# Kernel tuning notes

Measured on AMD Instinct MI355X. Metric: run time of the kernel, lower is better.

Reference implementation:

```python
import jax, jax.numpy as jnp
import numpy as np

BS, L, D, N = 4, 2048, 1024, 16

def setup_inputs() -> dict:
    key = jax.random.key(0)
    ks = jax.random.split(key, 8)
    s = 1.0 / np.sqrt(D)
    x  = jax.random.normal(ks[0], (BS, L, D), dtype=jnp.float32)
    # torch Linear params; stored transposed so y = x @ W + b
    W1 = jax.random.uniform(ks[1], (D, D), jnp.float32, -s, s)
    b1 = jax.random.uniform(ks[2], (D,),   jnp.float32, -s, s)
    W2 = jax.random.uniform(ks[3], (D, N), jnp.float32, -s, s)
    b2 = jax.random.uniform(ks[4], (N,),   jnp.float32, -s, s)
    W3 = jax.random.uniform(ks[5], (D, N), jnp.float32, -s, s)
    b3 = jax.random.uniform(ks[6], (N,),   jnp.float32, -s, s)
    A  = jax.random.normal(ks[7], (D, N),  jnp.float32) * np.sqrt(2.0 / (D + N))  # xavier
    return {"x": x, "W1": W1, "b1": b1, "W2": W2, "b2": b2, "W3": W3, "b3": b3, "A": A}

def reference(x, W1, b1, W2, b2, W3, b3, A):
    # S6 forward (non-recurrent branch).
    B = x @ W2 + b2                     # (b,l,n)
    C = x @ W3 + b3                     # (b,l,n)
    delta = jax.nn.softplus(x @ W1 + b1)  # (b,l,d)
    # dA = exp(einsum('bld,dn->bldn', delta, A)) is multiplied by an all-zero h
    # in the original forward, so it does not affect the output (dead code under DCE).
    dB = jnp.einsum('bld,bln->bldn', delta, B)   # (b,l,d,n) -- 512 MB intermediate
    h = x[..., None] * dB                         # (b,l,d,n)
    y = jnp.einsum('bln,bldn->bld', C, h)         # (b,l,d)
    return y
```

## Files before the change

### kernel.cpp

```cpp
#include <hip/hip_runtime.h>
#include <hip/hip_bf16.h>
#include <math.h>


namespace {

constexpr int Dd   = 1024;
constexpr int ROWS = 8192;

typedef __bf16 bf16x8 __attribute__((ext_vector_type(8)));
typedef float  floatx4 __attribute__((ext_vector_type(4)));

__device__ __forceinline__ float softplus_fast(float v) {
    float l = __logf(1.0f + __expf(v));
    return v > 15.0f ? v : l;
}
__device__ __forceinline__ float bf_lo(unsigned short u) {
    union { unsigned q; float f; } c; c.q = ((unsigned)u) << 16; return c.f;
}

__device__ __forceinline__ void gld_lds16(const __bf16* g, __bf16* l) {
    __builtin_amdgcn_global_load_lds(
        (const __attribute__((address_space(1))) void*)g,
        (__attribute__((address_space(3))) void*)l, 16, 0, 0);
}

#define BAR()    asm volatile("s_barrier" ::: "memory")
#define LGKM0()  asm volatile("s_waitcnt lgkmcnt(0)" ::: "memory")
#define VMCNT(n) asm volatile("s_waitcnt vmcnt(" #n ")" ::: "memory")

__global__ __launch_bounds__(256) void w23_kernel(
    const float* __restrict__ W2, const float* __restrict__ W3,
    __bf16* __restrict__ W2t, __bf16* __restrict__ W3t)
{
    const int t  = threadIdx.x;
    const int n  = t >> 4;
    const int k0 = blockIdx.x * 64 + (t & 15) * 4;
    ushort4 a, b;
    union { __bf16 h; unsigned short u; } c;
    c.h = (__bf16)W2[(size_t)(k0 + 0) * 16 + n]; a.x = c.u;
    c.h = (__bf16)W2[(size_t)(k0 + 1) * 16 + n]; a.y = c.u;
    c.h = (__bf16)W2[(size_t)(k0 + 2) * 16 + n]; a.z = c.u;
    c.h = (__bf16)W2[(size_t)(k0 + 3) * 16 + n]; a.w = c.u;
    c.h = (__bf16)W3[(size_t)(k0 + 0) * 16 + n]; b.x = c.u;
    c.h = (__bf16)W3[(size_t)(k0 + 1) * 16 + n]; b.y = c.u;
    c.h = (__bf16)W3[(size_t)(k0 + 2) * 16 + n]; b.z = c.u;
    c.h = (__bf16)W3[(size_t)(k0 + 3) * 16 + n]; b.w = c.u;
    *(ushort4*)&W2t[(size_t)n * Dd + k0] = a;
    *(ushort4*)&W3t[(size_t)n * Dd + k0] = b;
}

__global__ __launch_bounds__(256, 4) void prep_kernel(
    const float* __restrict__ X, const float* __restrict__ W1,
    const __bf16* __restrict__ W2t, const float* __restrict__ b2,
    const __bf16* __restrict__ W3t, const float* __restrict__ b3,
    __bf16* __restrict__ Xb, __bf16* __restrict__ W1t, float* __restrict__ Sv)
{
    const int t = threadIdx.x;

    if (blockIdx.x >= 512) {
        __shared__ __bf16 tile[64][66];
        const int bidx = blockIdx.x - 512;
        const int bi = bidx >> 4, bj = bidx & 15;
        const int c = t & 63, r4 = t >> 6;
        #pragma unroll
        for (int i = 0; i < 16; ++i) {
            const int r = i * 4 + r4;
            tile[r][c] = (__bf16)W1[(size_t)(bi * 64 + r) * Dd + bj * 64 + c];
        }
        __syncthreads();
        #pragma unroll
        for (int i = 0; i < 16; ++i) {
            const int r = i * 4 + r4;
            W1t[(size_t)(bj * 64 + r) * Dd + bi * 64 + c] = tile[c][r];
        }
        return;
    }

    __shared__ float red[4][2][16][16];
    const int w = t >> 6, lane = t & 63;
    const int l15 = lane & 15, quad = lane >> 4;
    const int row0 = blockIdx.x * 16;
    const int kw = w * 256;
    const size_t xoff = (size_t)(row0 + l15) * Dd;
    const size_t woff = (size_t)l15 * Dd;

    floatx4 acc0 = {0.f, 0.f, 0.f, 0.f}, acc1 = {0.f, 0.f, 0.f, 0.f};
    #pragma unroll
    for (int ks = 0; ks < 8; ++ks) {
        const int k0 = kw + ks * 32 + quad * 8;
        const float4 xa = *(const float4*)&X[xoff + k0];
        const float4 xb = *(const float4*)&X[xoff + k0 + 4];
        bf16x8 af;
        af[0] = (__bf16)xa.x; af[1] = (__bf16)xa.y;
        af[2] = (__bf16)xa.z; af[3] = (__bf16)xa.w;
        af[4] = (__bf16)xb.x; af[5] = (__bf16)xb.y;
        af[6] = (__bf16)xb.z; af[7] = (__bf16)xb.w;
        *(bf16x8*)&Xb[xoff + k0] = af;
        const bf16x8 w2f = *(const bf16x8*)&W2t[woff + k0];
        const bf16x8 w3f = *(const bf16x8*)&W3t[woff + k0];
        acc0 = __builtin_amdgcn_mfma_f32_16x16x32_bf16(af, w2f, acc0, 0, 0, 0);
        acc1 = __builtin_amdgcn_mfma_f32_16x16x32_bf16(af, w3f, acc1, 0, 0, 0);
    }
    #pragma unroll
    for (int r = 0; r < 4; ++r) {
        red[w][0][quad * 4 + r][l15] = acc0[r];
        red[w][1][quad * 4 + r][l15] = acc1[r];
    }
    __syncthreads();
    {
        const int r = t >> 4, n = t & 15;
        float B = b2[n], C = b3[n];
        #pragma unroll
        for (int ww = 0; ww < 4; ++ww) {
            B += red[ww][0][r][n];
            C += red[ww][1][r][n];
        }
        float p = B * C;
        p += __shfl_xor(p, 1); p += __shfl_xor(p, 2);
        p += __shfl_xor(p, 4); p += __shfl_xor(p, 8);
        if (n == 0) Sv[row0 + r] = p;
    }
}

#define MF(mt, nt, a_, b_) \
    acc[mt][nt] = __builtin_amdgcn_mfma_f32_16x16x32_bf16(a_, b_, acc[mt][nt], 0, 0, 0)
#define MFMA8(mb) do { \
    __builtin_amdgcn_s_setprio(1); \
    MF(mb + 0, 0, af0, bf0); MF(mb + 0, 1, af0, bf1); \
    MF(mb + 1, 0, af1, bf0); MF(mb + 1, 1, af1, bf1); \
    MF(mb + 2, 0, af2, bf0); MF(mb + 2, 1, af2, bf1); \
    MF(mb + 3, 0, af3, bf0); MF(mb + 3, 1, af3, bf1); \
    __builtin_amdgcn_s_setprio(0); } while (0)

#define TILE(B0_, B1_, NX1_, KA_, KB_, S1_, S2_, N1_, N2_) do { \
    bf16x8 af0, af1, af2, af3, bf0, bf1; \
     \
    af0 = rdA(B0_, 0); af1 = rdA(B0_, 1); af2 = rdA(B0_, 2); af3 = rdA(B0_, 3); \
    bf0 = rdB(B0_, 0); bf1 = rdB(B0_, 1); \
    if (S1_) { stageA(NX1_, KA_); stageB(NX1_, KA_); } \
    BAR(); LGKM0(); MFMA8(0); BAR(); \
     \
    af0 = rdA(B0_, 4); af1 = rdA(B0_, 5); af2 = rdA(B0_, 6); af3 = rdA(B0_, 7); \
    BAR(); LGKM0(); MFMA8(4); VMCNT(N1_); BAR(); \
     \
    af0 = rdA(B1_, 0); af1 = rdA(B1_, 1); af2 = rdA(B1_, 2); af3 = rdA(B1_, 3); \
    bf0 = rdB(B1_, 0); bf1 = rdB(B1_, 1); \
    if (S2_) { stageA(B0_, KB_); stageB(B0_, KB_); } \
    BAR(); LGKM0(); MFMA8(0); BAR(); \
     \
    af0 = rdA(B1_, 4); af1 = rdA(B1_, 5); af2 = rdA(B1_, 6); af3 = rdA(B1_, 7); \
    BAR(); LGKM0(); MFMA8(4); VMCNT(N2_); BAR(); \
} while (0)

__global__ __launch_bounds__(512, 2) void gemm_kernel(
    const __bf16* __restrict__ Xb, const __bf16* __restrict__ W1t,
    const float* __restrict__ Sv, const float* __restrict__ b1,
    float* __restrict__ Y)
{
    __shared__ __attribute__((aligned(16))) __bf16 lds[73728];
    const int t = threadIdx.x, lane = t & 63;
    const int w = t >> 6, wm = w & 1, wn = w >> 1;
    const int l15 = lane & 15, quad = lane >> 4;
    const int cb = blockIdx.x & 7, rb = blockIdx.x >> 3;
    const int row0 = rb * 256, col0 = cb * 128;

    floatx4 acc[8][2] = {};

    const __bf16* gAs[2]; int dAs[2];
    #pragma unroll
    for (int i = 0; i < 2; ++i) {
        const int d = i * 512 + t, r = d >> 2, cp = d & 3, c = cp ^ ((r >> 1) & 3);
        gAs[i] = Xb + (size_t)(row0 + r) * Dd + c * 8;
        dAs[i] = d * 8;
    }
    const __bf16* gBs; int dBs;
    {
        const int d = t, r = d >> 2, cp = d & 3, c = cp ^ ((r >> 1) & 3);
        gBs = W1t + (size_t)(col0 + r) * Dd + c * 8;
        dBs = d * 8;
    }

    auto stageA = [&](int slot, int kb) {
        #pragma unroll
        for (int i = 0; i < 2; ++i)
            gld_lds16(gAs[i] + kb, &lds[slot * 8192 + dAs[i]]);
    };
    auto stageB = [&](int slot, int kb) {
        gld_lds16(gBs + kb, &lds[49152 + slot * 4096 + dBs]);
    };

    const int sc  = (quad ^ ((l15 >> 1) & 3)) * 8;
    const int aro = (wm * 128 + l15) * 32 + sc;
    const int bro = (wn * 32 + l15) * 32 + sc;

    auto rdA = [&](int slot, int mt) {
        return *(const bf16x8*)&lds[slot * 8192 + aro + mt * 512];
    };
    auto rdB = [&](int slot, int nt) {
        return *(const bf16x8*)&lds[49152 + slot * 4096 + bro + nt * 512];
    };

    stageA(0, 0);   stageB(0, 0);
    stageA(1, 32);  stageB(1, 32);
    stageA(2, 64);  stageB(2, 64);
    stageA(3, 96);  stageB(3, 96);
    stageA(4, 128); stageB(4, 128);
    VMCNT(12); BAR();

    int um3 = 0;
    #pragma unroll 1
    for (int u = 0; u <= 12; ++u) {
        const int b0 = um3 * 2, b1v = b0 + 1;
        const int nx1 = (um3 == 0) ? 5 : (um3 == 1) ? 1 : 3;
        TILE(b0, b1v, nx1, (u + 2) * 64 + 32, (u + 3) * 64, true, true, 12, 12);
        um3 = (um3 == 2) ? 0 : um3 + 1;
    }
    TILE(2, 3, 1, 992, 0, true,  false, 12, 9);
    TILE(4, 5, 3, 0,   0, false, false, 6,  3);
    TILE(0, 1, 5, 0,   0, false, false, 0,  0);

    float bias[2];
    #pragma unroll
    for (int nt = 0; nt < 2; ++nt) bias[nt] = b1[col0 + wn * 32 + nt * 16 + l15];

    #pragma unroll
    for (int mt = 0; mt < 8; ++mt) {
        #pragma unroll
        for (int rr = 0; rr < 4; ++rr) {
            const int row = row0 + wm * 128 + mt * 16 + quad * 4 + rr;
            const float sv = Sv[row];
            const unsigned short* xrow =
                (const unsigned short*)(Xb + (size_t)row * Dd + col0);
            float* yrow = Y + (size_t)row * Dd + col0;
            #pragma unroll
            for (int nt = 0; nt < 2; ++nt) {
                const int cl = wn * 32 + nt * 16 + l15;
                const float v  = acc[mt][nt][rr] + bias[nt];
                const float sp = softplus_fast(v);
                yrow[cl] = bf_lo(xrow[cl]) * sp * sv;
            }
        }
    }
}

}

extern "C" void kernel_launch(void* const* d_in, const int* in_sizes, int n_in,
                              void* d_out, int out_size, void* d_ws, size_t ws_size,
                              hipStream_t stream)
{
    const float* X  = (const float*)d_in[0];
    const float* W1 = (const float*)d_in[1];
    const float* b1 = (const float*)d_in[2];
    const float* W2 = (const float*)d_in[3];
    const float* b2 = (const float*)d_in[4];
    const float* W3 = (const float*)d_in[5];
    const float* b3 = (const float*)d_in[6];
    float* Y = (float*)d_out;

    char* ws = (char*)d_ws;
    __bf16* Xb  = (__bf16*)ws;
    __bf16* W1t = (__bf16*)(ws + 16777216);
    float*  Sv  = (float*) (ws + 16777216 + 2097152);
    __bf16* W2t = (__bf16*)(ws + 16777216 + 2097152 + 32768);
    __bf16* W3t = (__bf16*)(ws + 16777216 + 2097152 + 65536);

    hipLaunchKernelGGL(w23_kernel, dim3(16), dim3(256), 0, stream, W2, W3, W2t, W3t);
    hipLaunchKernelGGL(prep_kernel, dim3(768), dim3(256), 0, stream,
                       X, W1, W2t, b2, W3t, b3, Xb, W1t, Sv);
    hipLaunchKernelGGL(gemm_kernel, dim3((ROWS / 256) * (Dd / 128)), dim3(512), 0, stream,
                       Xb, W1t, Sv, b1, Y);
}
```

Before: 136.1 us.

## Reshape warp tiling to 4x2 waves with 64x64 per-wave tiles

Changes the 8-wave layout from 2x4 (128x32 per wave) to 4x2 (64x64 per wave), so each wave issues 16 MFMAs per k-step from 4 A and 4 B fragments. Each k-step now has one MFMA phase instead of two, which halves the barrier count and cuts the LDS fragment reads per MFMA. The main loop is also restructured to unroll three tiles per iteration, removing the modulo slot bookkeeping. The cost is more B fragment registers, which may put pressure on occupancy.

```diff
diff --git a/kernel.cpp b/kernel.cpp
--- a/kernel.cpp
+++ b/kernel.cpp
@@ -125,32 +125,26 @@
 
 #define MF(mt, nt, a_, b_) \
     acc[mt][nt] = __builtin_amdgcn_mfma_f32_16x16x32_bf16(a_, b_, acc[mt][nt], 0, 0, 0)
-#define MFMA8(mb) do { \
+#define MFMA16() do { \
     __builtin_amdgcn_s_setprio(1); \
-    MF(mb + 0, 0, af0, bf0); MF(mb + 0, 1, af0, bf1); \
-    MF(mb + 1, 0, af1, bf0); MF(mb + 1, 1, af1, bf1); \
-    MF(mb + 2, 0, af2, bf0); MF(mb + 2, 1, af2, bf1); \
-    MF(mb + 3, 0, af3, bf0); MF(mb + 3, 1, af3, bf1); \
+    MF(0, 0, af0, bf0); MF(0, 1, af0, bf1); MF(0, 2, af0, bf2); MF(0, 3, af0, bf3); \
+    MF(1, 0, af1, bf0); MF(1, 1, af1, bf1); MF(1, 2, af1, bf2); MF(1, 3, af1, bf3); \
+    MF(2, 0, af2, bf0); MF(2, 1, af2, bf1); MF(2, 2, af2, bf2); MF(2, 3, af2, bf3); \
+    MF(3, 0, af3, bf0); MF(3, 1, af3, bf1); MF(3, 2, af3, bf2); MF(3, 3, af3, bf3); \
     __builtin_amdgcn_s_setprio(0); } while (0)
 
 #define TILE(B0_, B1_, NX1_, KA_, KB_, S1_, S2_, N1_, N2_) do { \
-    bf16x8 af0, af1, af2, af3, bf0, bf1; \
+    bf16x8 af0, af1, af2, af3, bf0, bf1, bf2, bf3; \
      \
     af0 = rdA(B0_, 0); af1 = rdA(B0_, 1); af2 = rdA(B0_, 2); af3 = rdA(B0_, 3); \
-    bf0 = rdB(B0_, 0); bf1 = rdB(B0_, 1); \
+    bf0 = rdB(B0_, 0); bf1 = rdB(B0_, 1); bf2 = rdB(B0_, 2); bf3 = rdB(B0_, 3); \
     if (S1_) { stageA(NX1_, KA_); stageB(NX1_, KA_); } \
-    BAR(); LGKM0(); MFMA8(0); BAR(); \
-     \
-    af0 = rdA(B0_, 4); af1 = rdA(B0_, 5); af2 = rdA(B0_, 6); af3 = rdA(B0_, 7); \
-    BAR(); LGKM0(); MFMA8(4); VMCNT(N1_); BAR(); \
+    BAR(); LGKM0(); MFMA16(); VMCNT(N1_); BAR(); \
      \
     af0 = rdA(B1_, 0); af1 = rdA(B1_, 1); af2 = rdA(B1_, 2); af3 = rdA(B1_, 3); \
-    bf0 = rdB(B1_, 0); bf1 = rdB(B1_, 1); \
+    bf0 = rdB(B1_, 0); bf1 = rdB(B1_, 1); bf2 = rdB(B1_, 2); bf3 = rdB(B1_, 3); \
     if (S2_) { stageA(B0_, KB_); stageB(B0_, KB_); } \
-    BAR(); LGKM0(); MFMA8(0); BAR(); \
-     \
-    af0 = rdA(B1_, 4); af1 = rdA(B1_, 5); af2 = rdA(B1_, 6); af3 = rdA(B1_, 7); \
-    BAR(); LGKM0(); MFMA8(4); VMCNT(N2_); BAR(); \
+    BAR(); LGKM0(); MFMA16(); VMCNT(N2_); BAR(); \
 } while (0)
 
 __global__ __launch_bounds__(512, 2) void gemm_kernel(
@@ -160,12 +154,12 @@
 {
     __shared__ __attribute__((aligned(16))) __bf16 lds[73728];
     const int t = threadIdx.x, lane = t & 63;
-    const int w = t >> 6, wm = w & 1, wn = w >> 1;
+    const int w = t >> 6, wm = w & 3, wn = w >> 2;
     const int l15 = lane & 15, quad = lane >> 4;
     const int cb = blockIdx.x & 7, rb = blockIdx.x >> 3;
     const int row0 = rb * 256, col0 = cb * 128;
 
-    floatx4 acc[8][2] = {};
+    floatx4 acc[4][4] = {};
 
     const __bf16* gAs[2]; int dAs[2];
     #pragma unroll
@@ -191,8 +185,8 @@
     };
 
     const int sc  = (quad ^ ((l15 >> 1) & 3)) * 8;
-    const int aro = (wm * 128 + l15) * 32 + sc;
-    const int bro = (wn * 32 + l15) * 32 + sc;
+    const int aro = (wm * 64 + l15) * 32 + sc;
+    const int bro = (wn * 64 + l15) * 32 + sc;
 
     auto rdA = [&](int slot, int mt) {
         return *(const bf16x8*)&lds[slot * 8192 + aro + mt * 512];
@@ -208,34 +202,34 @@
     stageA(4, 128); stageB(4, 128);
     VMCNT(12); BAR();
 
-    int um3 = 0;
     #pragma unroll 1
-    for (int u = 0; u <= 12; ++u) {
-        const int b0 = um3 * 2, b1v = b0 + 1;
-        const int nx1 = (um3 == 0) ? 5 : (um3 == 1) ? 1 : 3;
-        TILE(b0, b1v, nx1, (u + 2) * 64 + 32, (u + 3) * 64, true, true, 12, 12);
-        um3 = (um3 == 2) ? 0 : um3 + 1;
-    }
-    TILE(2, 3, 1, 992, 0, true,  false, 12, 9);
-    TILE(4, 5, 3, 0,   0, false, false, 6,  3);
-    TILE(0, 1, 5, 0,   0, false, false, 0,  0);
-
-    float bias[2];
-    #pragma unroll
-    for (int nt = 0; nt < 2; ++nt) bias[nt] = b1[col0 + wn * 32 + nt * 16 + l15];
-
-    #pragma unroll
-    for (int mt = 0; mt < 8; ++mt) {
+    for (int uu = 0; uu < 4; ++uu) {
+        const int ku = uu * 192;
+        TILE(0, 1, 5, ku + 160, ku + 192, true, true, 12, 12);
+        TILE(2, 3, 1, ku + 224, ku + 256, true, true, 12, 12);
+        TILE(4, 5, 3, ku + 288, ku + 320, true, true, 12, 12);
+    }
+    TILE(0, 1, 5, 928, 960, true,  true,  12, 12);
+    TILE(2, 3, 1, 992, 0,   true,  false, 12, 9);
+    TILE(4, 5, 3, 0,   0,   false, false, 6,  3);
+    TILE(0, 1, 5, 0,   0,   false, false, 0,  0);
+
+    float bias[4];
+    #pragma unroll
+    for (int nt = 0; nt < 4; ++nt) bias[nt] = b1[col0 + wn * 64 + nt * 16 + l15];
+
+    #pragma unroll
+    for (int mt = 0; mt < 4; ++mt) {
         #pragma unroll
         for (int rr = 0; rr < 4; ++rr) {
-            const int row = row0 + wm * 128 + mt * 16 + quad * 4 + rr;
+            const int row = row0 + wm * 64 + mt * 16 + quad * 4 + rr;
             const float sv = Sv[row];
             const unsigned short* xrow =
                 (const unsigned short*)(Xb + (size_t)row * Dd + col0);
             float* yrow = Y + (size_t)row * Dd + col0;
             #pragma unroll
-            for (int nt = 0; nt < 2; ++nt) {
-                const int cl = wn * 32 + nt * 16 + l15;
+            for (int nt = 0; nt < 4; ++nt) {
+                const int cl = wn * 64 + nt * 16 + l15;
                 const float v  = acc[mt][nt][rr] + bias[nt];
                 const float sp = softplus_fast(v);
                 yrow[cl] = bf_lo(xrow[cl]) * sp * sv;
```

After: 132.7 us. 2.5% less time.
